# Kernel optimization log

Measured on AMD Instinct MI355X. Metric: run time of the kernel, lower is better.

The kernel has to match this reference:

```python
import jax, jax.numpy as jnp
import numpy as np

EPS = 1e-4

def _ema(unit_embeddings, unit_confidence, unit_mask):
    # unit_embeddings: (B, J, D), unit_confidence/unit_mask: (B, J)
    emb_j = jnp.swapaxes(unit_embeddings, 0, 1)        # (J, B, D)
    p_j = jnp.swapaxes(unit_confidence, 0, 1)          # (J, B)
    m_j = jnp.swapaxes(unit_mask, 0, 1)                # (J, B)

    B, _, D = unit_embeddings.shape
    prev0 = jnp.zeros((B, D), dtype=unit_embeddings.dtype)

    def step(prev, inp):
        emb, p, m = inp                                # (B,D), (B,), (B,)
        p = jnp.clip(p, EPS, 1.0 - EPS)[:, None]       # (B,1)
        m = m[:, None]                                 # (B,1)
        cur = jnp.where(m, emb, jnp.zeros_like(emb))
        new = jnp.where(m, p * cur + (1.0 - p) * prev, prev)
        return new, new

    _, smoothed = jax.lax.scan(step, prev0, (emb_j, p_j, m_j))  # (J, B, D)
    return jnp.swapaxes(smoothed, 0, 1)                # (B, J, D)

def _upsample(smoothed, boundary_mask):
    # smoothed: (B, J, D), boundary_mask: (B, L) bool
    J = smoothed.shape[1]
    idx = jnp.cumsum(boundary_mask.astype(jnp.int32), axis=1) - 1
    idx = jnp.clip(idx, 0, J - 1)                      # (B, L)
    return jnp.take_along_axis(smoothed, idx[:, :, None], axis=1)  # (B, L, D)

def setup_inputs() -> dict:
    key = jax.random.key(0)
    k1, k2, k3, k4 = jax.random.split(key, 4)
    B, J, L, D = 16, 1024, 4096, 512
    unit_embeddings = jax.random.normal(k1, (B, J, D), dtype=jnp.float32)
    unit_confidence = jax.random.uniform(k2, (B, J), dtype=jnp.float32)
    unit_mask = jax.random.randint(k3, (B, J), 0, 2).astype(bool)
    boundary_mask = jax.random.randint(k4, (B, L), 0, 2).astype(bool)
    return {
        "unit_embeddings": unit_embeddings,
        "unit_confidence": unit_confidence,
        "unit_mask": unit_mask,
        "boundary_mask": boundary_mask,
    }

def reference(unit_embeddings, unit_confidence, unit_mask, boundary_mask):
    smoothed = _ema(unit_embeddings, unit_confidence, unit_mask)
    frames = _upsample(smoothed, boundary_mask)
    return frames
```

## Files before the change

### kernel.cpp

```cpp
#include <hip/hip_runtime.h>
#include <cstddef>

namespace {
constexpr int Bn = 16;
constexpr int Jn = 1024;
constexpr int Ln = 4096;
constexpr int Dn = 512;
constexpr int G  = 32;
constexpr int C  = Jn / G;
constexpr float kEps = 1e-4f;
constexpr int PASS1_BLOCKS = Bn * C;
}

__global__ __launch_bounds__(128) void k_fused1(
    const float* __restrict__ emb, const float* __restrict__ conf,
    const int* __restrict__ mask, const int* __restrict__ bnd,
    float* __restrict__ local, float* __restrict__ E,
    float* __restrict__ PA, float* __restrict__ Ap, int* __restrict__ idx) {
  int blk = blockIdx.x;
  int t = threadIdx.x;
  if (blk < PASS1_BLOCKS) {
    int b = blk / C, c = blk % C;
    int base = b * Jn + c * G;
    float4 s = make_float4(0.f, 0.f, 0.f, 0.f);
    float prod = 1.0f;
#pragma unroll 8
    for (int i = 0; i < G; ++i) {
      int j = base + i;
      float p = conf[j];
      p = fminf(fmaxf(p, kEps), 1.0f - kEps);
      bool m = (mask[j] != 0);
      float q = 1.0f - p;
      float4 e = ((const float4*)(emb + (size_t)j * Dn))[t];
      if (m) {
        s.x = p * e.x + q * s.x;
        s.y = p * e.y + q * s.y;
        s.z = p * e.z + q * s.z;
        s.w = p * e.w + q * s.w;
        prod *= q;
      }
      ((float4*)(local + (size_t)j * Dn))[t] = s;
      if (t == 0) PA[j] = prod;
    }
    ((float4*)(E + (size_t)blk * Dn))[t] = s;
    if (t == 0) Ap[blk] = prod;
  } else {
    int b = blk - PASS1_BLOCKS;
    const int per = Ln / 128;
    const int* row = bnd + (size_t)b * Ln;
    int s = 0;
#pragma unroll 8
    for (int i = 0; i < per; ++i) s += (row[t * per + i] != 0) ? 1 : 0;

    __shared__ int sh[128];
    sh[t] = s;
    __syncthreads();
    for (int off = 1; off < 128; off <<= 1) {
      int v = (t >= off) ? sh[t - off] : 0;
      __syncthreads();
      sh[t] += v;
      __syncthreads();
    }
    int run = sh[t] - s;
#pragma unroll 8
    for (int i = 0; i < per; ++i) {
      run += (row[t * per + i] != 0) ? 1 : 0;
      int v = run - 1;
      v = v < 0 ? 0 : (v > Jn - 1 ? Jn - 1 : v);
      idx[(size_t)b * Ln + t * per + i] = v;
    }
  }
}

__global__ __launch_bounds__(64) void k_chunk_start(
    const float* __restrict__ E, const float* __restrict__ Ap,
    float* __restrict__ S) {
  int tg = blockIdx.x * 64 + threadIdx.x;
  int b = tg / (Dn / 4), d4 = tg % (Dn / 4);
  float4 s = make_float4(0.f, 0.f, 0.f, 0.f);
#pragma unroll 8
  for (int c = 0; c < C; ++c) {
    ((float4*)(S + ((size_t)(b * C + c)) * Dn))[d4] = s;
    float a = Ap[b * C + c];
    float4 e = ((const float4*)(E + ((size_t)(b * C + c)) * Dn))[d4];
    s.x = e.x + a * s.x;
    s.y = e.y + a * s.y;
    s.z = e.z + a * s.z;
    s.w = e.w + a * s.w;
  }
}

__global__ __launch_bounds__(256) void k_gather(
    const float* __restrict__ local, const float* __restrict__ PA,
    const float* __restrict__ S, const int* __restrict__ idx,
    float* __restrict__ out) {
  unsigned bid = blockIdx.x;
  unsigned sb = (bid & 7u) * 4096u + (bid >> 3);
  size_t tid = (size_t)sb * 256 + threadIdx.x;
  int d4 = (int)(tid & (Dn / 4 - 1));
  size_t bl = tid >> 7;
  int j = idx[bl];
  size_t b = bl >> 12;
  int c = j >> 5;
  float pa = PA[b * Jn + (size_t)j];
  float4 sc = ((const float4*)(S + (b * C + (size_t)c) * Dn))[d4];
  float4 lo = ((const float4*)(local + (b * Jn + (size_t)j) * Dn))[d4];
  float4 o;
  o.x = lo.x + pa * sc.x;
  o.y = lo.y + pa * sc.y;
  o.z = lo.z + pa * sc.z;
  o.w = lo.w + pa * sc.w;
  ((float4*)out)[tid] = o;
}

extern "C" void kernel_launch(void* const* d_in, const int* in_sizes, int n_in,
                              void* d_out, int out_size, void* d_ws, size_t ws_size,
                              hipStream_t stream) {
  const float* emb  = (const float*)d_in[0];
  const float* conf = (const float*)d_in[1];
  const int*   mask = (const int*)d_in[2];
  const int*   bnd  = (const int*)d_in[3];
  float* out = (float*)d_out;

  float* ws = (float*)d_ws;
  float* local = ws;
  float* E   = local + (size_t)Bn * Jn * Dn;
  float* S   = E + (size_t)Bn * C * Dn;
  float* PA  = S + (size_t)Bn * C * Dn;
  float* Ap  = PA + (size_t)Bn * Jn;
  int*   idx = (int*)(Ap + Bn * C);

  hipLaunchKernelGGL(k_fused1, dim3(PASS1_BLOCKS + Bn), dim3(128), 0, stream,
                     emb, conf, mask, bnd, local, E, PA, Ap, idx);
  hipLaunchKernelGGL(k_chunk_start, dim3(Bn * (Dn / 4) / 64), dim3(64), 0, stream,
                     E, Ap, S);
  size_t total4 = (size_t)Bn * Ln * (Dn / 4);
  hipLaunchKernelGGL(k_gather, dim3((unsigned)(total4 / 256)), dim3(256), 0, stream,
                     local, PA, S, idx, out);
}
```

Measured before the change: 180.4 us.

## Store local scan results as bf16 and fuse chunk-start pass via last-block counter

```diff
diff --git a/kernel.cpp b/kernel.cpp
--- a/kernel.cpp
+++ b/kernel.cpp
@@ -12,11 +12,21 @@
 constexpr int PASS1_BLOCKS = Bn * C;
 }
 
+__device__ __forceinline__ unsigned short bf16rne(float x) {
+  unsigned u = __float_as_uint(x);
+  unsigned r = (u + 0x7fffu + ((u >> 16) & 1u)) >> 16;
+  return (unsigned short)r;
+}
+__device__ __forceinline__ float bf16tof(unsigned short h) {
+  return __uint_as_float(((unsigned)h) << 16);
+}
+
 __global__ __launch_bounds__(128) void k_fused1(
     const float* __restrict__ emb, const float* __restrict__ conf,
     const int* __restrict__ mask, const int* __restrict__ bnd,
-    float* __restrict__ local, float* __restrict__ E,
-    float* __restrict__ PA, float* __restrict__ Ap, int* __restrict__ idx) {
+    unsigned short* __restrict__ localh, float* __restrict__ E,
+    float* __restrict__ PA, float* __restrict__ Ap, float* __restrict__ S,
+    int* __restrict__ idx, int* __restrict__ cnt) {
   int blk = blockIdx.x;
   int t = threadIdx.x;
   if (blk < PASS1_BLOCKS) {
@@ -39,11 +49,33 @@
         s.w = p * e.w + q * s.w;
         prod *= q;
       }
-      ((float4*)(local + (size_t)j * Dn))[t] = s;
+      ushort4 h;
+      h.x = bf16rne(s.x); h.y = bf16rne(s.y);
+      h.z = bf16rne(s.z); h.w = bf16rne(s.w);
+      ((ushort4*)(localh + (size_t)j * Dn))[t] = h;
       if (t == 0) PA[j] = prod;
     }
     ((float4*)(E + (size_t)blk * Dn))[t] = s;
     if (t == 0) Ap[blk] = prod;
+
+    __threadfence();
+    __shared__ int who;
+    if (t == 0) who = atomicAdd(&cnt[b], 1);
+    __syncthreads();
+    if (who == C - 1) {
+      __threadfence();
+      float4 sv = make_float4(0.f, 0.f, 0.f, 0.f);
+#pragma unroll 8
+      for (int cc = 0; cc < C; ++cc) {
+        ((float4*)(S + ((size_t)(b * C + cc)) * Dn))[t] = sv;
+        float a = Ap[b * C + cc];
+        float4 ev = ((const float4*)(E + ((size_t)(b * C + cc)) * Dn))[t];
+        sv.x = ev.x + a * sv.x;
+        sv.y = ev.y + a * sv.y;
+        sv.z = ev.z + a * sv.z;
+        sv.w = ev.w + a * sv.w;
+      }
+    }
   } else {
     int b = blk - PASS1_BLOCKS;
     const int per = Ln / 128;
@@ -72,26 +104,8 @@
   }
 }
 
-__global__ __launch_bounds__(64) void k_chunk_start(
-    const float* __restrict__ E, const float* __restrict__ Ap,
-    float* __restrict__ S) {
-  int tg = blockIdx.x * 64 + threadIdx.x;
-  int b = tg / (Dn / 4), d4 = tg % (Dn / 4);
-  float4 s = make_float4(0.f, 0.f, 0.f, 0.f);
-#pragma unroll 8
-  for (int c = 0; c < C; ++c) {
-    ((float4*)(S + ((size_t)(b * C + c)) * Dn))[d4] = s;
-    float a = Ap[b * C + c];
-    float4 e = ((const float4*)(E + ((size_t)(b * C + c)) * Dn))[d4];
-    s.x = e.x + a * s.x;
-    s.y = e.y + a * s.y;
-    s.z = e.z + a * s.z;
-    s.w = e.w + a * s.w;
-  }
-}
-
 __global__ __launch_bounds__(256) void k_gather(
-    const float* __restrict__ local, const float* __restrict__ PA,
+    const unsigned short* __restrict__ localh, const float* __restrict__ PA,
     const float* __restrict__ S, const int* __restrict__ idx,
     float* __restrict__ out) {
   unsigned bid = blockIdx.x;
@@ -104,12 +118,12 @@
   int c = j >> 5;
   float pa = PA[b * Jn + (size_t)j];
   float4 sc = ((const float4*)(S + (b * C + (size_t)c) * Dn))[d4];
-  float4 lo = ((const float4*)(local + (b * Jn + (size_t)j) * Dn))[d4];
+  ushort4 lh = ((const ushort4*)(localh + (b * Jn + (size_t)j) * Dn))[d4];
   float4 o;
-  o.x = lo.x + pa * sc.x;
-  o.y = lo.y + pa * sc.y;
-  o.z = lo.z + pa * sc.z;
-  o.w = lo.w + pa * sc.w;
+  o.x = bf16tof(lh.x) + pa * sc.x;
+  o.y = bf16tof(lh.y) + pa * sc.y;
+  o.z = bf16tof(lh.z) + pa * sc.z;
+  o.w = bf16tof(lh.w) + pa * sc.w;
   ((float4*)out)[tid] = o;
 }
 
@@ -123,18 +137,18 @@
   float* out = (float*)d_out;
 
   float* ws = (float*)d_ws;
-  float* local = ws;
-  float* E   = local + (size_t)Bn * Jn * Dn;
+  unsigned short* localh = (unsigned short*)ws;
+  float* E   = ws + (size_t)Bn * Jn * Dn / 2;
   float* S   = E + (size_t)Bn * C * Dn;
   float* PA  = S + (size_t)Bn * C * Dn;
   float* Ap  = PA + (size_t)Bn * Jn;
   int*   idx = (int*)(Ap + Bn * C);
+  int*   cnt = idx + (size_t)Bn * Ln;
 
+  hipMemsetAsync(cnt, 0, Bn * sizeof(int), stream);
   hipLaunchKernelGGL(k_fused1, dim3(PASS1_BLOCKS + Bn), dim3(128), 0, stream,
-                     emb, conf, mask, bnd, local, E, PA, Ap, idx);
-  hipLaunchKernelGGL(k_chunk_start, dim3(Bn * (Dn / 4) / 64), dim3(64), 0, stream,
-                     E, Ap, S);
+                     emb, conf, mask, bnd, localh, E, PA, Ap, S, idx, cnt);
   size_t total4 = (size_t)Bn * Ln * (Dn / 4);
   hipLaunchKernelGGL(k_gather, dim3((unsigned)(total4 / 256)), dim3(256), 0, stream,
-                     local, PA, S, idx, out);
+                     localh, PA, S, idx, out);
 }
```

After: 224.7 us. +24.6%, slower.
